# Kernel optimization log

Hardware: AMD Instinct MI355X
Metric: run time of the kernel (lower is better)

## Reference

```python
import jax, jax.numpy as jnp
import numpy as np
from functools import partial

SIZES = (32.0, 64.0, 128.0, 256.0, 512.0)
RATIOS = (0.5, 1.0, 2.0)
POS_T, NEG_T = 0.7, 0.3


def _make_anchors(img_size, grid_sizes):
    # Mirrors AnchorGenerator: per feature, per size, per ratio, grid-flattened.
    parts = []
    for g in grid_sizes:
        stride = img_size / g
        steps = jnp.arange(g, dtype=jnp.float32) * stride
        x, y = jnp.meshgrid(steps, steps, indexing='ij')  # torch default 'ij'
        for s in SIZES:
            for r in RATIOS:
                rs = float(np.sqrt(r))
                wa = jnp.full((g, g), s * rs, jnp.float32)
                ha = jnp.full((g, g), s / rs, jnp.float32)
                parts.append(jnp.stack((x, y, wa, ha), axis=-1).reshape(-1, 4))
    return jnp.concatenate(parts, axis=0)  # [R,4] (cx,cy,w,h)


def _conv(x, w, b, pad):
    y = jax.lax.conv_general_dilated(x, w, (1, 1), [(pad, pad), (pad, pad)],
                                     dimension_numbers=('NCHW', 'OIHW', 'NCHW'))
    return y + b[None, :, None, None]


def _head(feat, conv_w, conv_b, cls_w, cls_b, box_w, box_b):
    t = jax.nn.relu(_conv(feat, conv_w, conv_b, 1))
    logits = _conv(t, cls_w, cls_b, 0)   # [b,A,g,g]
    bbox = _conv(t, box_w, box_b, 0)     # [b,4A,g,g]
    b, A, g, _ = logits.shape
    logits = logits.reshape(b, -1)       # [b, A*g*g] (anchor-major, matches anchor order)
    bbox = bbox.reshape(b, A, 4, g, g).transpose(0, 1, 3, 4, 2).reshape(b, -1, 4)
    return logits, bbox


def _iou(a, b):
    # a [R,4] xyxy, b [N,4] xyxy -> [R,N]
    lt = jnp.maximum(a[:, None, :2], b[None, :, :2])
    rb = jnp.minimum(a[:, None, 2:], b[None, :, 2:])
    wh = jnp.clip(rb - lt, 0.0)
    inter = wh[..., 0] * wh[..., 1]
    area_a = (a[:, 2] - a[:, 0]) * (a[:, 3] - a[:, 1])
    area_b = (b[:, 2] - b[:, 0]) * (b[:, 3] - b[:, 1])
    return inter / (area_a[:, None] + area_b[None, :] - inter)


def _label_one(anchors_xyxy, gt_xywh):
    # label_anchors for a single image
    gt = jnp.concatenate([gt_xywh[:, :2], gt_xywh[:, :2] + gt_xywh[:, 2:]], axis=-1)
    iou = _iou(anchors_xyxy, gt)               # [R,N]
    score = iou.max(axis=1)
    matched = gt[jnp.argmax(iou, axis=1)]      # [R,4]
    pos = score > POS_T
    pos = pos.at[jnp.argmax(iou, axis=0)].set(True)  # best anchor per gt
    labels = jnp.where(score < NEG_T, 0.0, jnp.where(pos, 1.0, -1.0))
    return labels, matched


def _forward(images, feats, gt_boxes, conv_w, conv_b, cls_w, cls_b, box_w, box_b):
    grid_sizes = [f.shape[-1] for f in feats]
    anchors = _make_anchors(float(images.shape[-1]), grid_sizes)  # [R,4] cwh
    half = anchors[:, 2:] * 0.5
    anchors_xyxy = jnp.concatenate([anchors[:, :2] - half, anchors[:, :2] + half], -1)
    outs = [_head(f, conv_w, conv_b, cls_w, cls_b, box_w, box_b) for f in feats]
    obj = jnp.concatenate([o for o, _ in outs], axis=1)      # [b,R]
    deltas = jnp.concatenate([d for _, d in outs], axis=1)   # [b,R,4]
    labels, matched = jax.vmap(partial(_label_one, anchors_xyxy))(gt_boxes)
    preds = jnp.concatenate([obj[..., None], deltas], axis=-1)  # [b,R,5]
    return preds, labels, matched


def setup_inputs() -> dict:
    key = jax.random.key(0)
    ks = jax.random.split(key, 12)
    b, C, A = 2, 256, 15
    grids = (128, 64, 32, 16, 8)
    inp = {'images': jax.random.uniform(ks[0], (b, 3, 512, 512), jnp.float32)}
    for i, g in enumerate(grids):
        inp[f'feat{i}'] = jax.random.normal(ks[1 + i], (b, C, g, g), jnp.float32)
    xy = jax.random.uniform(ks[6], (b, 32, 2), jnp.float32) * 384.0
    wh = 16.0 + jax.random.uniform(ks[7], (b, 32, 2), jnp.float32) * 112.0
    inp['gt_boxes'] = jnp.concatenate([xy, wh], axis=-1)  # (x,y,w,h)
    inp['conv_w'] = 0.01 * jax.random.normal(ks[8], (C, C, 3, 3), jnp.float32)
    inp['conv_b'] = jnp.zeros((C,), jnp.float32)
    inp['cls_w'] = 0.01 * jax.random.normal(ks[9], (A, C, 1, 1), jnp.float32)
    inp['cls_b'] = jnp.zeros((A,), jnp.float32)
    inp['box_w'] = 0.01 * jax.random.normal(ks[10], (4 * A, C, 1, 1), jnp.float32)
    inp['box_b'] = jnp.zeros((4 * A,), jnp.float32)
    return inp


def reference(images, feat0, feat1, feat2, feat3, feat4, gt_boxes,
              conv_w, conv_b, cls_w, cls_b, box_w, box_b):
    return _forward(images, [feat0, feat1, feat2, feat3, feat4], gt_boxes,
                    conv_w, conv_b, cls_w, cls_b, box_w, box_b)
```

## Files before the change

### kernel.cpp

```cpp
#include <hip/hip_runtime.h>

typedef unsigned short u16;
typedef unsigned char  u8;
typedef unsigned int   u32;
typedef __bf16 bf16x8 __attribute__((ext_vector_type(8)));
typedef float  f32x4  __attribute__((ext_vector_type(4)));
typedef u16    u16x8  __attribute__((ext_vector_type(8)));
typedef u16    u16x4  __attribute__((ext_vector_type(4)));

#define R_TOTAL 327360
#define LAB_OFF 3273600
#define MAT_OFF 3928320

static __device__ const int    D_LOG2G[5] = {7, 6, 5, 4, 3};
static __device__ const size_t D_FTOFF[5] = {0, 8389120, 10486784, 11011584, 11143168};
static __device__ const int    D_TPOFF[5] = {0, 32768, 40960, 43008, 43520};
static __device__ const int    D_AOFF[5]  = {0, 245760, 307200, 322560, 326400};

static __device__ const float D_WH[15][2] = {
  {22.627416997969522f, 45.254833995939045f}, {32.f, 32.f},   {45.254833995939045f, 22.627416997969522f},
  {45.254833995939045f, 90.50966799187809f},  {64.f, 64.f},   {90.50966799187809f, 45.254833995939045f},
  {90.50966799187809f, 181.01933598375618f},  {128.f, 128.f}, {181.01933598375618f, 90.50966799187809f},
  {181.01933598375618f, 362.03867196751236f}, {256.f, 256.f}, {362.03867196751236f, 181.01933598375618f},
  {362.03867196751236f, 724.0773439350247f},  {512.f, 512.f}, {724.0773439350247f, 362.03867196751236f},
};

__device__ __forceinline__ u16 f2bf(float x) {
  u32 u = __float_as_uint(x);
  u32 r = u + 0x7FFFu + ((u >> 16) & 1u);
  return (u16)(r >> 16);
}
__device__ __forceinline__ float bf2f(u16 v) { return __uint_as_float(((u32)v) << 16); }

__device__ __forceinline__ void glds16(const void* g, void* l) {
  __builtin_amdgcn_global_load_lds(
      (const __attribute__((address_space(1))) u32*)g,
      (__attribute__((address_space(3))) u32*)l, 16, 0, 0);
}

__device__ inline void anchor_box(int r, float& x1, float& y1, float& x2, float& y2) {
  #pragma clang fp contract(off)
  int off, lg;
  if (r < 245760)      { off = 0;      lg = 7; }
  else if (r < 307200) { off = 245760; lg = 6; }
  else if (r < 322560) { off = 307200; lg = 5; }
  else if (r < 326400) { off = 322560; lg = 4; }
  else                 { off = 326400; lg = 3; }
  int rem  = r - off;
  int a    = rem >> (2 * lg);
  int rem2 = rem & ((1 << (2 * lg)) - 1);
  int i = rem2 >> lg;
  int j = rem2 & ((1 << lg) - 1);
  float stride = (float)(512 >> lg);
  float cx = (float)i * stride;
  float cy = (float)j * stride;
  float hw = D_WH[a][0] * 0.5f;
  float hh = D_WH[a][1] * 0.5f;
  x1 = cx - hw; y1 = cy - hh; x2 = cx + hw; y2 = cy + hh;
}

__device__ inline float iou_f(float ax1, float ay1, float ax2, float ay2,
                              float bx1, float by1, float bx2, float by2) {
  #pragma clang fp contract(off)
  float ltx = fmaxf(ax1, bx1), lty = fmaxf(ay1, by1);
  float rbx = fminf(ax2, bx2), rby = fminf(ay2, by2);
  float iw = fmaxf(rbx - ltx, 0.f);
  float ih = fmaxf(rby - lty, 0.f);
  float inter = iw * ih;
  float aa = (ax2 - ax1) * (ay2 - ay1);
  float ab = (bx2 - bx1) * (by2 - by1);
  return inter / (aa + ab - inter);
}

__global__ __launch_bounds__(256) void pack_w_kernel(const float* __restrict__ cw,
                                                     u16* __restrict__ wp) {
  int idx = blockIdx.x * 256 + threadIdx.x;
  int ks  = idx >> 13;
  int rem = idx & 8191;
  int co  = rem >> 5;
  int k   = rem & 31;
  int tap = ks >> 3;
  int cb  = ks & 7;
  float v = cw[co * 2304 + (cb * 32 + k) * 9 + tap];
  int qd = k >> 3, wi = k & 7;
  int dq = qd ^ ((co >> 1) & 3);
  wp[(size_t)ks * 8192 + co * 32 + dq * 8 + wi] = f2bf(v);
}

__global__ __launch_bounds__(256) void pack_head_w(
    const float* __restrict__ cls_w, const float* __restrict__ cls_b,
    const float* __restrict__ box_w, const float* __restrict__ box_b,
    u16* __restrict__ Wb, float* __restrict__ hbias) {
  int idx = blockIdx.x * 256 + threadIdx.x;
  int row = idx >> 8, k = idx & 255;
  float v = (row < 15) ? cls_w[row * 256 + k] : (row < 75) ? box_w[(row - 15) * 256 + k] : 0.f;
  Wb[row * 256 + k] = f2bf(v);
  if (idx < 80) hbias[idx] = (idx < 15) ? cls_b[idx] : (idx < 75) ? box_b[idx - 15] : 0.f;
}

__global__ __launch_bounds__(256) void feat_pack_kernel(
    const float* __restrict__ f0, const float* __restrict__ f1,
    const float* __restrict__ f2, const float* __restrict__ f3,
    const float* __restrict__ f4, u16* __restrict__ Ft) {
  __shared__ float tile[64][65];
  int bid = blockIdx.x;
  int l, base, nb1;
  if (bid < 514)      { l = 0; base = 0;   nb1 = 257; }
  else if (bid < 644) { l = 1; base = 514; nb1 = 65; }
  else if (bid < 678) { l = 2; base = 644; nb1 = 17; }
  else if (bid < 688) { l = 3; base = 678; nb1 = 5; }
  else                { l = 4; base = 688; nb1 = 2; }
  const int lg = D_LOG2G[l];
  const int HW = 1 << (2 * lg);
  int blk = bid - base;
  int b   = blk / nb1;
  int p0  = (blk - b * nb1) * 64;
  u16* dst = Ft + D_FTOFF[l];
  const int tid = threadIdx.x;
  if (p0 >= HW) {
    if (tid < 32) {
      u16x8 z = (u16x8)0;
      *(u16x8*)(dst + ((size_t)b * (HW + 1) + HW) * 256 + tid * 8) = z;
    }
    return;
  }
  const float* fsel = (l == 0) ? f0 : (l == 1) ? f1 : (l == 2) ? f2 : (l == 3) ? f3 : f4;
  const float* fb = fsel + (size_t)b * 256 * HW;
  for (int cg = 0; cg < 4; ++cg) {
    __syncthreads();
    #pragma unroll
    for (int i = 0; i < 16; ++i) {
      int idx = i * 256 + tid;
      int cl = idx >> 6, pp = idx & 63;
      tile[cl][pp] = fb[(size_t)(cg * 64 + cl) * HW + p0 + pp];
    }
    __syncthreads();
    #pragma unroll
    for (int i = 0; i < 2; ++i) {
      int slot = i * 256 + tid;
      int pos = slot >> 3, ch = slot & 7;
      u16x8 v;
      #pragma unroll
      for (int j = 0; j < 8; ++j) v[j] = f2bf(tile[ch * 8 + j][pos]);
      *(u16x8*)(dst + ((size_t)b * (HW + 1) + p0 + pos) * 256 + cg * 64 + ch * 8) = v;
    }
  }
}

__global__ __launch_bounds__(128) void conv_mfma_kernel(
    const u16* __restrict__ Ft, const u16* __restrict__ wp,
    const float* __restrict__ cb, u16* __restrict__ tP) {
  __shared__ __align__(16) u8 Asb[8192];
  __shared__ __align__(16) u8 Bsb[4096];
  const int bid = blockIdx.x;
  int l, base;
  if (bid < 1024)      { l = 0; base = 0; }
  else if (bid < 1280) { l = 1; base = 1024; }
  else if (bid < 1344) { l = 2; base = 1280; }
  else if (bid < 1360) { l = 3; base = 1344; }
  else                 { l = 4; base = 1360; }
  const int lg = D_LOG2G[l];
  const int g = 1 << lg, HW = 1 << (2 * lg);
  const int lognt = 2 * lg - 5;
  const int blk = bid - base;
  const int ct = blk >> lognt;
  const int tile = blk & ((1 << lognt) - 1);
  const int n0 = tile << 6;
  const int co0 = ct << 7;
  const int tid = threadIdx.x;
  const int wv = tid >> 6, lane = tid & 63;
  const u16* FtL = Ft + D_FTOFF[l];
  const u8* wpb = (const u8*)wp;
  const int b_img = n0 >> (2 * lg);
  const int dq = tid & 3;
  const int nl0 = tid >> 2, nl1 = nl0 + 32;
  const int swz0 = (dq ^ ((nl0 >> 1) & 3)) << 3;
  const int swz1 = (dq ^ ((nl1 >> 1) & 3)) << 3;
  const int pg0 = (n0 + nl0) & (HW - 1);
  const int h0 = pg0 >> lg, w0 = pg0 & (g - 1);
  const int pg1 = (n0 + nl1) & (HW - 1);
  const int h1 = pg1 >> lg, w1 = pg1 & (g - 1);
  const u16* bimg = FtL + (size_t)b_img * (HW + 1) * 256;
  const int lm = lane & 15, lq = lane >> 4;
  int aoffs[4], boffs[4];
  #pragma unroll
  for (int mi = 0; mi < 4; ++mi) {
    int row = wv * 64 + mi * 16 + lm;
    aoffs[mi] = row * 64 + ((lq ^ ((row >> 1) & 3)) << 4);
  }
  #pragma unroll
  for (int ni = 0; ni < 4; ++ni) {
    int col = ni * 16 + lm;
    boffs[ni] = col * 64 + ((lq ^ ((col >> 1) & 3)) << 4);
  }
  f32x4 acc[4][4];
  #pragma unroll
  for (int mi = 0; mi < 4; ++mi)
    #pragma unroll
    for (int ni = 0; ni < 4; ++ni) acc[mi][ni] = (f32x4)0.f;

  for (int tap = 0; tap < 9; ++tap) {
    const int dh = tap / 3 - 1, dw = tap % 3 - 1;
    int sh0 = h0 + dh, sw0 = w0 + dw;
    int r0 = ((unsigned)sh0 < (unsigned)g && (unsigned)sw0 < (unsigned)g) ? (sh0 * g + sw0) : HW;
    int sh1 = h1 + dh, sw1 = w1 + dw;
    int r1 = ((unsigned)sh1 < (unsigned)g && (unsigned)sw1 < (unsigned)g) ? (sh1 * g + sw1) : HW;
    const u16* src0 = bimg + (size_t)r0 * 256 + swz0;
    const u16* src1 = bimg + (size_t)r1 * 256 + swz1;
    const u8* aS = wpb + (size_t)(tap * 8) * 16384 + co0 * 64;
    for (int cb8 = 0; cb8 < 8; ++cb8) {
      __syncthreads();
      glds16(src0 + cb8 * 32, Bsb + wv * 1024);
      glds16(src1 + cb8 * 32, Bsb + (2 + wv) * 1024);
      const u8* aK = aS + (size_t)cb8 * 16384;
      #pragma unroll
      for (int c = 0; c < 4; ++c) {
        int ch = c * 2 + wv;
        glds16(aK + ch * 1024 + lane * 16, Asb + ch * 1024);
      }
      __syncthreads();
      bf16x8 af[4], bfr[4];
      #pragma unroll
      for (int mi = 0; mi < 4; ++mi) af[mi] = *(const bf16x8*)(Asb + aoffs[mi]);
      #pragma unroll
      for (int ni = 0; ni < 4; ++ni) bfr[ni] = *(const bf16x8*)(Bsb + boffs[ni]);
      #pragma unroll
      for (int mi = 0; mi < 4; ++mi)
        #pragma unroll
        for (int ni = 0; ni < 4; ++ni)
          acc[mi][ni] = __builtin_amdgcn_mfma_f32_16x16x32_bf16(af[mi], bfr[ni], acc[mi][ni], 0, 0, 0);
    }
  }
  u16* tPL = tP + ((size_t)D_TPOFF[l] + (size_t)b_img * HW) * 256;
  #pragma unroll
  for (int mi = 0; mi < 4; ++mi) {
    const int cob = co0 + wv * 64 + mi * 16 + lq * 4;
    const float4 bs = *(const float4*)&cb[cob];
    #pragma unroll
    for (int ni = 0; ni < 4; ++ni) {
      int pp = (n0 + ni * 16 + lm) & (HW - 1);
      u16x4 v;
      v[0] = f2bf(fmaxf(acc[mi][ni][0] + bs.x, 0.f));
      v[1] = f2bf(fmaxf(acc[mi][ni][1] + bs.y, 0.f));
      v[2] = f2bf(fmaxf(acc[mi][ni][2] + bs.z, 0.f));
      v[3] = f2bf(fmaxf(acc[mi][ni][3] + bs.w, 0.f));
      *(u16x4*)&tPL[(size_t)pp * 256 + cob] = v;
    }
  }
}

__global__ __launch_bounds__(128) void head_mfma_kernel(
    const u16* __restrict__ tP, const u16* __restrict__ Wb,
    const float* __restrict__ hbias, float* __restrict__ out) {
  __shared__ __align__(16) u8 Bsb[32768];
  const int bid = blockIdx.x;
  int l, base;
  if (bid < 512)      { l = 0; base = 0; }
  else if (bid < 640) { l = 1; base = 512; }
  else if (bid < 672) { l = 2; base = 640; }
  else if (bid < 680) { l = 3; base = 672; }
  else                { l = 4; base = 680; }
  const int lg = D_LOG2G[l];
  const int HW = 1 << (2 * lg);
  const int blk = bid - base;
  const int n0 = blk << 6;
  const int tid = threadIdx.x;
  const int wv = tid >> 6, lane = tid & 63;
  const int lm = lane & 15, lq = lane >> 4;
  const u16* src = tP + ((size_t)D_TPOFF[l] + n0) * 256;
  #pragma unroll
  for (int i = 0; i < 16; ++i) {
    int c = wv + i * 2;
    int slot = c * 64 + lane;
    int pos = slot >> 5, sp = slot & 31;
    glds16(src + (size_t)pos * 256 + ((sp ^ (pos & 7)) << 3), Bsb + c * 1024);
  }
  __syncthreads();
  f32x4 acc[5][2];
  #pragma unroll
  for (int mi = 0; mi < 5; ++mi) { acc[mi][0] = (f32x4)0.f; acc[mi][1] = (f32x4)0.f; }
  for (int kb = 0; kb < 8; ++kb) {
    bf16x8 af[5], bfr[2];
    #pragma unroll
    for (int mi = 0; mi < 5; ++mi)
      af[mi] = *(const bf16x8*)&Wb[(mi * 16 + lm) * 256 + kb * 32 + lq * 8];
    #pragma unroll
    for (int ni = 0; ni < 2; ++ni) {
      int p_ = wv * 32 + ni * 16 + lm;
      bfr[ni] = *(const bf16x8*)(Bsb + p_ * 512 + (((kb * 4 + lq) ^ (p_ & 7)) << 4));
    }
    #pragma unroll
    for (int mi = 0; mi < 5; ++mi)
      #pragma unroll
      for (int ni = 0; ni < 2; ++ni)
        acc[mi][ni] = __builtin_amdgcn_mfma_f32_16x16x32_bf16(af[mi], bfr[ni], acc[mi][ni], 0, 0, 0);
  }
  const int b   = n0 >> (2 * lg);
  const int pgb = n0 & (HW - 1);
  const size_t obase = (size_t)b * R_TOTAL;
  const int aoff = D_AOFF[l];
  #pragma unroll
  for (int mi = 0; mi < 5; ++mi) {
    #pragma unroll
    for (int r = 0; r < 4; ++r) {
      int oc = mi * 16 + lq * 4 + r;
      if (oc < 75) {
        float bs = hbias[oc];
        size_t rr; int comp;
        if (oc < 15) { rr = (size_t)aoff + (size_t)oc * HW; comp = 0; }
        else { int o2 = oc - 15; rr = (size_t)aoff + (size_t)(o2 >> 2) * HW; comp = 1 + (o2 & 3); }
        #pragma unroll
        for (int ni = 0; ni < 2; ++ni) {
          int pg = pgb + wv * 32 + ni * 16 + lm;
          out[(obase + rr + pg) * 5 + comp] = acc[mi][ni][r] + bs;
        }
      }
    }
  }
}

__global__ __launch_bounds__(256) void label_kernel(const float* __restrict__ gt,
                                                    float* __restrict__ out) {
  #pragma clang fp contract(off)
  __shared__ float gx[32][4];
  const int b = blockIdx.y;
  const int tid = threadIdx.x;
  if (tid < 32) {
    const float* gp = gt + ((size_t)b * 32 + tid) * 4;
    float x = gp[0], y = gp[1], w = gp[2], h = gp[3];
    gx[tid][0] = x; gx[tid][1] = y; gx[tid][2] = x + w; gx[tid][3] = y + h;
  }
  __syncthreads();
  int r = blockIdx.x * 256 + tid;
  if (r >= R_TOTAL) return;
  float ax1, ay1, ax2, ay2;
  anchor_box(r, ax1, ay1, ax2, ay2);
  float best = -1e30f; int bi = 0;
  for (int n = 0; n < 32; ++n) {
    float v = iou_f(ax1, ay1, ax2, ay2, gx[n][0], gx[n][1], gx[n][2], gx[n][3]);
    if (v > best) { best = v; bi = n; }
  }
  float lab = (best < 0.3f) ? 0.f : ((best > 0.7f) ? 1.f : -1.f);
  out[LAB_OFF + (size_t)b * R_TOTAL + r] = lab;
  float4 m; m.x = gx[bi][0]; m.y = gx[bi][1]; m.z = gx[bi][2]; m.w = gx[bi][3];
  *(float4*)&out[MAT_OFF + ((size_t)b * R_TOTAL + r) * 4] = m;
}

__global__ __launch_bounds__(256) void argmax_part_kernel(const float* __restrict__ gt,
                                                          float2* __restrict__ part) {
  #pragma clang fp contract(off)
  const int bn = blockIdx.x >> 3, chunk = blockIdx.x & 7;
  const int b = bn >> 5, n = bn & 31;
  const float* gp = gt + ((size_t)b * 32 + n) * 4;
  const float bx1 = gp[0], by1 = gp[1];
  const float bx2 = bx1 + gp[2], by2 = by1 + gp[3];
  const int r0 = chunk * 40920;
  float best = -1e30f; int bi = 0;
  for (int r = r0 + threadIdx.x; r < r0 + 40920; r += 256) {
    float ax1, ay1, ax2, ay2;
    anchor_box(r, ax1, ay1, ax2, ay2);
    float v = iou_f(ax1, ay1, ax2, ay2, bx1, by1, bx2, by2);
    if (v > best) { best = v; bi = r; }
  }
  __shared__ float sv[256];
  __shared__ int   si[256];
  sv[threadIdx.x] = best; si[threadIdx.x] = bi;
  __syncthreads();
  for (int s = 128; s > 0; s >>= 1) {
    if ((int)threadIdx.x < s) {
      float v2 = sv[threadIdx.x + s]; int i2 = si[threadIdx.x + s];
      float v1 = sv[threadIdx.x];     int i1 = si[threadIdx.x];
      if (v2 > v1 || (v2 == v1 && i2 < i1)) { sv[threadIdx.x] = v2; si[threadIdx.x] = i2; }
    }
    __syncthreads();
  }
  if (threadIdx.x == 0) part[blockIdx.x] = make_float2(sv[0], __int_as_float(si[0]));
}

__global__ __launch_bounds__(64) void argmax_final_kernel(const float* __restrict__ gt,
                                                          const float2* __restrict__ part,
                                                          float* __restrict__ out) {
  #pragma clang fp contract(off)
  const int t = threadIdx.x;
  if (t >= 64) return;
  const int b = t >> 5;
  float best = -1e30f; int bi = 0;
  for (int c = 0; c < 8; ++c) {
    float2 pv = part[t * 8 + c];
    if (pv.x > best) { best = pv.x; bi = __float_as_int(pv.y); }
  }
  float ax1, ay1, ax2, ay2;
  anchor_box(bi, ax1, ay1, ax2, ay2);
  float score = -1e30f;
  for (int n2 = 0; n2 < 32; ++n2) {
    const float* gp = gt + ((size_t)b * 32 + n2) * 4;
    float v = iou_f(ax1, ay1, ax2, ay2, gp[0], gp[1], gp[0] + gp[2], gp[1] + gp[3]);
    score = fmaxf(score, v);
  }
  out[LAB_OFF + (size_t)b * R_TOTAL + bi] = (score < 0.3f) ? 0.f : 1.f;
}

extern "C" void kernel_launch(void* const* d_in, const int* in_sizes, int n_in,
                              void* d_out, int out_size, void* d_ws, size_t ws_size,
                              hipStream_t stream) {
  const float* f0     = (const float*)d_in[1];
  const float* f1     = (const float*)d_in[2];
  const float* f2     = (const float*)d_in[3];
  const float* f3     = (const float*)d_in[4];
  const float* f4     = (const float*)d_in[5];
  const float* gt     = (const float*)d_in[6];
  const float* conv_w = (const float*)d_in[7];
  const float* conv_b = (const float*)d_in[8];
  const float* cls_w  = (const float*)d_in[9];
  const float* cls_b  = (const float*)d_in[10];
  const float* box_w  = (const float*)d_in[11];
  const float* box_b  = (const float*)d_in[12];
  float* out = (float*)d_out;
  u8* wsb = (u8*)d_ws;

  u16*   wp    = (u16*)wsb;
  u16*   Ft    = (u16*)(wsb + 1179648);
  u16*   tP    = (u16*)(wsb + 23532544);
  u16*   Wb    = (u16*)(wsb + 45880320);
  float* hbias = (float*)(wsb + 45921280);
  float2* part = (float2*)(wsb + 45921600);

  pack_w_kernel<<<2304, 256, 0, stream>>>(conv_w, wp);
  pack_head_w<<<80, 256, 0, stream>>>(cls_w, cls_b, box_w, box_b, Wb, hbias);
  feat_pack_kernel<<<692, 256, 0, stream>>>(f0, f1, f2, f3, f4, Ft);
  conv_mfma_kernel<<<1364, 128, 0, stream>>>(Ft, wp, conv_b, tP);
  head_mfma_kernel<<<682, 128, 0, stream>>>(tP, Wb, hbias, out);
  label_kernel<<<dim3(1279, 2), 256, 0, stream>>>(gt, out);
  argmax_part_kernel<<<512, 256, 0, stream>>>(gt, part);
  argmax_final_kernel<<<1, 64, 0, stream>>>(gt, part, out);
}
```

Baseline: 270.4 us.

## Double-buffer conv LDS staging, fuse label with argmax partials, merge weight packs

The conv MFMA kernel now double-buffers its A/B LDS tiles. It issues the next k-slice's global-to-LDS loads before computing the current one, which removes one barrier per step and overlaps loads with MFMA work. The per-anchor IoU pass also records per-block best-anchor partials for each GT box in shared memory. This replaces the separate argmax pass that recomputed all 327k IoUs per GT, with a small final reduction kernel. The two weight-pack kernels are merged into one launch. Costs are double the LDS in conv (lower occupancy is possible) and a large shared array in the label kernel.

After: 231.6 us. 1.17x faster.

```diff
diff --git a/kernel.cpp b/kernel.cpp
--- a/kernel.cpp
+++ b/kernel.cpp
@@ -11,6 +11,7 @@
 #define R_TOTAL 327360
 #define LAB_OFF 3273600
 #define MAT_OFF 3928320
+#define NLBLK   1279
 
 static __device__ const int    D_LOG2G[5] = {7, 6, 5, 4, 3};
 static __device__ const size_t D_FTOFF[5] = {0, 8389120, 10486784, 11011584, 11143168};
@@ -72,30 +73,30 @@
   return inter / (aa + ab - inter);
 }
 
-__global__ __launch_bounds__(256) void pack_w_kernel(const float* __restrict__ cw,
-                                                     u16* __restrict__ wp) {
-  int idx = blockIdx.x * 256 + threadIdx.x;
-  int ks  = idx >> 13;
-  int rem = idx & 8191;
-  int co  = rem >> 5;
-  int k   = rem & 31;
-  int tap = ks >> 3;
-  int cb  = ks & 7;
-  float v = cw[co * 2304 + (cb * 32 + k) * 9 + tap];
-  int qd = k >> 3, wi = k & 7;
-  int dq = qd ^ ((co >> 1) & 3);
-  wp[(size_t)ks * 8192 + co * 32 + dq * 8 + wi] = f2bf(v);
-}
-
-__global__ __launch_bounds__(256) void pack_head_w(
+__global__ __launch_bounds__(256) void pack_all_kernel(
+    const float* __restrict__ cw, u16* __restrict__ wp,
     const float* __restrict__ cls_w, const float* __restrict__ cls_b,
     const float* __restrict__ box_w, const float* __restrict__ box_b,
     u16* __restrict__ Wb, float* __restrict__ hbias) {
-  int idx = blockIdx.x * 256 + threadIdx.x;
-  int row = idx >> 8, k = idx & 255;
-  float v = (row < 15) ? cls_w[row * 256 + k] : (row < 75) ? box_w[(row - 15) * 256 + k] : 0.f;
-  Wb[row * 256 + k] = f2bf(v);
-  if (idx < 80) hbias[idx] = (idx < 15) ? cls_b[idx] : (idx < 75) ? box_b[idx - 15] : 0.f;
+  if (blockIdx.x < 2304) {
+    int idx = blockIdx.x * 256 + threadIdx.x;
+    int ks  = idx >> 13;
+    int rem = idx & 8191;
+    int co  = rem >> 5;
+    int k   = rem & 31;
+    int tap = ks >> 3;
+    int cb  = ks & 7;
+    float v = cw[co * 2304 + (cb * 32 + k) * 9 + tap];
+    int qd = k >> 3, wi = k & 7;
+    int dq = qd ^ ((co >> 1) & 3);
+    wp[(size_t)ks * 8192 + co * 32 + dq * 8 + wi] = f2bf(v);
+  } else {
+    int idx = (blockIdx.x - 2304) * 256 + threadIdx.x;
+    int row = idx >> 8, k = idx & 255;
+    float v = (row < 15) ? cls_w[row * 256 + k] : (row < 75) ? box_w[(row - 15) * 256 + k] : 0.f;
+    Wb[row * 256 + k] = f2bf(v);
+    if (idx < 80) hbias[idx] = (idx < 15) ? cls_b[idx] : (idx < 75) ? box_b[idx - 15] : 0.f;
+  }
 }
 
 __global__ __launch_bounds__(256) void feat_pack_kernel(
@@ -150,8 +151,8 @@
 __global__ __launch_bounds__(128) void conv_mfma_kernel(
     const u16* __restrict__ Ft, const u16* __restrict__ wp,
     const float* __restrict__ cb, u16* __restrict__ tP) {
-  __shared__ __align__(16) u8 Asb[8192];
-  __shared__ __align__(16) u8 Bsb[4096];
+  __shared__ __align__(16) u8 Asb[16384];
+  __shared__ __align__(16) u8 Bsb[8192];
   const int bid = blockIdx.x;
   int l, base;
   if (bid < 1024)      { l = 0; base = 0; }
@@ -199,37 +200,55 @@
     #pragma unroll
     for (int ni = 0; ni < 4; ++ni) acc[mi][ni] = (f32x4)0.f;
 
-  for (int tap = 0; tap < 9; ++tap) {
+  auto tap_src = [&](int tap, const u16*& s0, const u16*& s1) {
     const int dh = tap / 3 - 1, dw = tap % 3 - 1;
     int sh0 = h0 + dh, sw0 = w0 + dw;
     int r0 = ((unsigned)sh0 < (unsigned)g && (unsigned)sw0 < (unsigned)g) ? (sh0 * g + sw0) : HW;
     int sh1 = h1 + dh, sw1 = w1 + dw;
     int r1 = ((unsigned)sh1 < (unsigned)g && (unsigned)sw1 < (unsigned)g) ? (sh1 * g + sw1) : HW;
-    const u16* src0 = bimg + (size_t)r0 * 256 + swz0;
-    const u16* src1 = bimg + (size_t)r1 * 256 + swz1;
-    const u8* aS = wpb + (size_t)(tap * 8) * 16384 + co0 * 64;
+    s0 = bimg + (size_t)r0 * 256 + swz0;
+    s1 = bimg + (size_t)r1 * 256 + swz1;
+  };
+  auto STAGE = [&](int p, int tap_, int cb8_, const u16* s0, const u16* s1) {
+    glds16(s0 + cb8_ * 32, Bsb + p * 4096 + wv * 1024);
+    glds16(s1 + cb8_ * 32, Bsb + p * 4096 + (2 + wv) * 1024);
+    const u8* aK = wpb + (size_t)(tap_ * 8 + cb8_) * 16384 + co0 * 64;
+    #pragma unroll
+    for (int c = 0; c < 4; ++c) {
+      int ch = c * 2 + wv;
+      glds16(aK + ch * 1024 + lane * 16, Asb + p * 8192 + ch * 1024);
+    }
+  };
+
+  const u16 *cs0, *cs1;
+  tap_src(0, cs0, cs1);
+  int p = 0;
+  STAGE(0, 0, 0, cs0, cs1);
+  __syncthreads();
+
+  for (int tap = 0; tap < 9; ++tap) {
+    const u16 *ns0 = cs0, *ns1 = cs1;
+    if (tap < 8) tap_src(tap + 1, ns0, ns1);
+    #pragma unroll
     for (int cb8 = 0; cb8 < 8; ++cb8) {
-      __syncthreads();
-      glds16(src0 + cb8 * 32, Bsb + wv * 1024);
-      glds16(src1 + cb8 * 32, Bsb + (2 + wv) * 1024);
-      const u8* aK = aS + (size_t)cb8 * 16384;
-      #pragma unroll
-      for (int c = 0; c < 4; ++c) {
-        int ch = c * 2 + wv;
-        glds16(aK + ch * 1024 + lane * 16, Asb + ch * 1024);
+      if (!(tap == 8 && cb8 == 7)) {
+        if (cb8 < 7) STAGE(p ^ 1, tap, cb8 + 1, cs0, cs1);
+        else         STAGE(p ^ 1, tap + 1, 0, ns0, ns1);
       }
-      __syncthreads();
       bf16x8 af[4], bfr[4];
       #pragma unroll
-      for (int mi = 0; mi < 4; ++mi) af[mi] = *(const bf16x8*)(Asb + aoffs[mi]);
+      for (int mi = 0; mi < 4; ++mi) af[mi] = *(const bf16x8*)(Asb + p * 8192 + aoffs[mi]);
       #pragma unroll
-      for (int ni = 0; ni < 4; ++ni) bfr[ni] = *(const bf16x8*)(Bsb + boffs[ni]);
+      for (int ni = 0; ni < 4; ++ni) bfr[ni] = *(const bf16x8*)(Bsb + p * 4096 + boffs[ni]);
       #pragma unroll
       for (int mi = 0; mi < 4; ++mi)
         #pragma unroll
         for (int ni = 0; ni < 4; ++ni)
           acc[mi][ni] = __builtin_amdgcn_mfma_f32_16x16x32_bf16(af[mi], bfr[ni], acc[mi][ni], 0, 0, 0);
-    }
+      __syncthreads();
+      p ^= 1;
+    }
+    cs0 = ns0; cs1 = ns1;
   }
   u16* tPL = tP + ((size_t)D_TPOFF[l] + (size_t)b_img * HW) * 256;
   #pragma unroll
@@ -319,10 +338,13 @@
   }
 }
 
-__global__ __launch_bounds__(256) void label_kernel(const float* __restrict__ gt,
-                                                    float* __restrict__ out) {
+__global__ __launch_bounds__(256) void label_fused_kernel(const float* __restrict__ gt,
+                                                          float* __restrict__ out,
+                                                          float2* __restrict__ partial) {
   #pragma clang fp contract(off)
   __shared__ float gx[32][4];
+  __shared__ float sh[256][33];
+  __shared__ float2 red[32][8];
   const int b = blockIdx.y;
   const int tid = threadIdx.x;
   if (tid < 32) {
@@ -331,73 +353,82 @@
     gx[tid][0] = x; gx[tid][1] = y; gx[tid][2] = x + w; gx[tid][3] = y + h;
   }
   __syncthreads();
-  int r = blockIdx.x * 256 + tid;
-  if (r >= R_TOTAL) return;
+  const int r = blockIdx.x * 256 + tid;
+  const bool valid = (r < R_TOTAL);
+  const int rv = valid ? r : 0;
   float ax1, ay1, ax2, ay2;
-  anchor_box(r, ax1, ay1, ax2, ay2);
+  anchor_box(rv, ax1, ay1, ax2, ay2);
   float best = -1e30f; int bi = 0;
   for (int n = 0; n < 32; ++n) {
     float v = iou_f(ax1, ay1, ax2, ay2, gx[n][0], gx[n][1], gx[n][2], gx[n][3]);
+    sh[tid][n] = valid ? v : -1e30f;
     if (v > best) { best = v; bi = n; }
   }
-  float lab = (best < 0.3f) ? 0.f : ((best > 0.7f) ? 1.f : -1.f);
-  out[LAB_OFF + (size_t)b * R_TOTAL + r] = lab;
-  float4 m; m.x = gx[bi][0]; m.y = gx[bi][1]; m.z = gx[bi][2]; m.w = gx[bi][3];
-  *(float4*)&out[MAT_OFF + ((size_t)b * R_TOTAL + r) * 4] = m;
-}
-
-__global__ __launch_bounds__(256) void argmax_part_kernel(const float* __restrict__ gt,
-                                                          float2* __restrict__ part) {
+  if (valid) {
+    float lab = (best < 0.3f) ? 0.f : ((best > 0.7f) ? 1.f : -1.f);
+    out[LAB_OFF + (size_t)b * R_TOTAL + r] = lab;
+    float4 m; m.x = gx[bi][0]; m.y = gx[bi][1]; m.z = gx[bi][2]; m.w = gx[bi][3];
+    *(float4*)&out[MAT_OFF + ((size_t)b * R_TOTAL + r) * 4] = m;
+  }
+  __syncthreads();
+  const int n = tid & 31, gr = tid >> 5;
+  float bv = -1e30f; int li = 0;
+  #pragma unroll 4
+  for (int a = 0; a < 32; ++a) {
+    int la = gr * 32 + a;
+    float v = sh[la][n];
+    if (v > bv) { bv = v; li = la; }
+  }
+  red[n][gr] = make_float2(bv, __int_as_float(li));
+  __syncthreads();
+  if (tid < 32) {
+    float fv = -1e30f; int fi = 0;
+    #pragma unroll
+    for (int g2 = 0; g2 < 8; ++g2) {
+      float2 pv = red[tid][g2];
+      int ii = __float_as_int(pv.y);
+      if (pv.x > fv) { fv = pv.x; fi = ii; }
+    }
+    partial[(size_t)(b * 32 + tid) * NLBLK + blockIdx.x] =
+        make_float2(fv, __int_as_float(blockIdx.x * 256 + fi));
+  }
+}
+
+__global__ __launch_bounds__(256) void argmax_final2_kernel(
+    const float* __restrict__ gt, const float2* __restrict__ partial,
+    float* __restrict__ out) {
   #pragma clang fp contract(off)
-  const int bn = blockIdx.x >> 3, chunk = blockIdx.x & 7;
-  const int b = bn >> 5, n = bn & 31;
-  const float* gp = gt + ((size_t)b * 32 + n) * 4;
-  const float bx1 = gp[0], by1 = gp[1];
-  const float bx2 = bx1 + gp[2], by2 = by1 + gp[3];
-  const int r0 = chunk * 40920;
-  float best = -1e30f; int bi = 0;
-  for (int r = r0 + threadIdx.x; r < r0 + 40920; r += 256) {
-    float ax1, ay1, ax2, ay2;
-    anchor_box(r, ax1, ay1, ax2, ay2);
-    float v = iou_f(ax1, ay1, ax2, ay2, bx1, by1, bx2, by2);
-    if (v > best) { best = v; bi = r; }
-  }
   __shared__ float sv[256];
   __shared__ int   si[256];
-  sv[threadIdx.x] = best; si[threadIdx.x] = bi;
+  const int b = blockIdx.x >> 5, n = blockIdx.x & 31;
+  const float2* pp = partial + (size_t)(b * 32 + n) * NLBLK;
+  const int tid = threadIdx.x;
+  float bv = -1e30f; int bi = 0x7fffffff;
+  for (int i = tid; i < NLBLK; i += 256) {
+    float2 pv = pp[i]; int ii = __float_as_int(pv.y);
+    if (pv.x > bv || (pv.x == bv && ii < bi)) { bv = pv.x; bi = ii; }
+  }
+  sv[tid] = bv; si[tid] = bi;
   __syncthreads();
   for (int s = 128; s > 0; s >>= 1) {
-    if ((int)threadIdx.x < s) {
-      float v2 = sv[threadIdx.x + s]; int i2 = si[threadIdx.x + s];
-      float v1 = sv[threadIdx.x];     int i1 = si[threadIdx.x];
-      if (v2 > v1 || (v2 == v1 && i2 < i1)) { sv[threadIdx.x] = v2; si[threadIdx.x] = i2; }
+    if (tid < s) {
+      float v2 = sv[tid + s]; int i2 = si[tid + s];
+      if (v2 > sv[tid] || (v2 == sv[tid] && i2 < si[tid])) { sv[tid] = v2; si[tid] = i2; }
     }
     __syncthreads();
   }
-  if (threadIdx.x == 0) part[blockIdx.x] = make_float2(sv[0], __int_as_float(si[0]));
-}
-
-__global__ __launch_bounds__(64) void argmax_final_kernel(const float* __restrict__ gt,
-                                                          const float2* __restrict__ part,
-                                                          float* __restrict__ out) {
-  #pragma clang fp contract(off)
-  const int t = threadIdx.x;
-  if (t >= 64) return;
-  const int b = t >> 5;
-  float best = -1e30f; int bi = 0;
-  for (int c = 0; c < 8; ++c) {
-    float2 pv = part[t * 8 + c];
-    if (pv.x > best) { best = pv.x; bi = __float_as_int(pv.y); }
-  }
-  float ax1, ay1, ax2, ay2;
-  anchor_box(bi, ax1, ay1, ax2, ay2);
-  float score = -1e30f;
-  for (int n2 = 0; n2 < 32; ++n2) {
-    const float* gp = gt + ((size_t)b * 32 + n2) * 4;
-    float v = iou_f(ax1, ay1, ax2, ay2, gp[0], gp[1], gp[0] + gp[2], gp[1] + gp[3]);
-    score = fmaxf(score, v);
-  }
-  out[LAB_OFF + (size_t)b * R_TOTAL + bi] = (score < 0.3f) ? 0.f : 1.f;
+  if (tid == 0) {
+    int banch = si[0];
+    float ax1, ay1, ax2, ay2;
+    anchor_box(banch, ax1, ay1, ax2, ay2);
+    float score = -1e30f;
+    for (int n2 = 0; n2 < 32; ++n2) {
+      const float* gp = gt + ((size_t)b * 32 + n2) * 4;
+      float v = iou_f(ax1, ay1, ax2, ay2, gp[0], gp[1], gp[0] + gp[2], gp[1] + gp[3]);
+      score = fmaxf(score, v);
+    }
+    out[LAB_OFF + (size_t)b * R_TOTAL + banch] = (score < 0.3f) ? 0.f : 1.f;
+  }
 }
 
 extern "C" void kernel_launch(void* const* d_in, const int* in_sizes, int n_in,
@@ -418,19 +449,17 @@
   float* out = (float*)d_out;
   u8* wsb = (u8*)d_ws;
 
-  u16*   wp    = (u16*)wsb;
-  u16*   Ft    = (u16*)(wsb + 1179648);
-  u16*   tP    = (u16*)(wsb + 23532544);
-  u16*   Wb    = (u16*)(wsb + 45880320);
-  float* hbias = (float*)(wsb + 45921280);
-  float2* part = (float2*)(wsb + 45921600);
-
-  pack_w_kernel<<<2304, 256, 0, stream>>>(conv_w, wp);
-  pack_head_w<<<80, 256, 0, stream>>>(cls_w, cls_b, box_w, box_b, Wb, hbias);
+  u16*    wp      = (u16*)wsb;
+  u16*    Ft      = (u16*)(wsb + 1179648);
+  u16*    tP      = (u16*)(wsb + 23532544);
+  u16*    Wb      = (u16*)(wsb + 45880320);
+  float*  hbias   = (float*)(wsb + 45921280);
+  float2* partial = (float2*)(wsb + 45921600);
+
+  pack_all_kernel<<<2384, 256, 0, stream>>>(conv_w, wp, cls_w, cls_b, box_w, box_b, Wb, hbias);
   feat_pack_kernel<<<692, 256, 0, stream>>>(f0, f1, f2, f3, f4, Ft);
   conv_mfma_kernel<<<1364, 128, 0, stream>>>(Ft, wp, conv_b, tP);
   head_mfma_kernel<<<682, 128, 0, stream>>>(tP, Wb, hbias, out);
-  label_kernel<<<dim3(1279, 2), 256, 0, stream>>>(gt, out);
-  argmax_part_kernel<<<512, 256, 0, stream>>>(gt, part);
-  argmax_final_kernel<<<1, 64, 0, stream>>>(gt, part, out);
-}
+  label_fused_kernel<<<dim3(NLBLK, 2), 256, 0, stream>>>(gt, out, partial);
+  argmax_final2_kernel<<<64, 256, 0, stream>>>(gt, partial, out);
+}
```
